# Optimization experiments

Hardware: AMD Instinct MI355X
Metric: run time of the kernel (lower is better)

## Reference

```python
import jax, jax.numpy as jnp
import numpy as np

NC = 1      # constants.nc (Game-of-Life grid channels)
GRID = 32
PAD_ITERS = 31


def _iterated_wrap_idx(n, p):
    # Faithfully simulate p iterations of circular pad-1 on a growing axis.
    # NOTE: this is NOT a single wrap-pad of p; the border alternates 0/n-1.
    idx = np.arange(n)
    for _ in range(p):
        idx = np.concatenate([idx[-1:], idx, idx[:1]])
    return jnp.asarray(idx)

_IDX = _iterated_wrap_idx(GRID, PAD_ITERS)  # length 94, static


def _pad(x):
    # one gather per spatial dim replaces the 31-iteration concat loop
    return x[:, :, _IDX][:, :, :, _IDX]


def _conv(x, w, b, stride):
    y = jax.lax.conv_general_dilated(
        x, w, window_strides=(stride, stride), padding='VALID',
        dimension_numbers=('NCHW', 'OIHW', 'NCHW'))
    return y + b[None, :, None, None]


def setup_inputs() -> dict:
    key = jax.random.key(0)
    ks = jax.random.split(key, 7)
    B = 16
    s_in = 1.0 / np.sqrt(NC * 32 * 32)      # fan-in init, keeps activations sane
    s_hid = 1.0 / np.sqrt(32 * 32 * 32)
    s_out = 1.0 / np.sqrt(32)
    return {
        'x': jax.random.normal(ks[0], (B, NC, GRID, GRID), jnp.float32),
        'in_w': jax.random.normal(ks[1], (32, NC, 32, 32), jnp.float32) * s_in,
        'in_b': jnp.zeros((32,), jnp.float32),
        'convs_w': jax.random.normal(ks[2], (20, 32, 32, 32, 32), jnp.float32) * s_hid,
        'convs_b': jnp.zeros((20, 32), jnp.float32),
        'out_w': jax.random.normal(ks[3], (NC, 32, 1, 1), jnp.float32) * s_out,
        'out_b': jnp.zeros((NC,), jnp.float32),
    }


def reference(x, in_w, in_b, convs_w, convs_b, out_w, out_b):
    # in_conv: pad(31 iters) + conv k=32 s=2 (no ReLU, as in original)
    h = _conv(_pad(x), in_w, in_b, 2)           # [B,32,32,32]

    def step(h, wb):
        w, b = wb
        h = jax.nn.relu(_conv(_pad(h), w, b, 2))
        return h, None

    h, _ = jax.lax.scan(step, h, (convs_w, convs_b))  # 20 hidden layers
    return _conv(h, out_w, out_b, 1)             # 1x1 out conv, no activation
```

## Files before the change

kernel.cpp:

```cpp
#include <hip/hip_runtime.h>


typedef _Float16 f16;
typedef _Float16 f16x8 __attribute__((ext_vector_type(8)));
typedef float f32x4 __attribute__((ext_vector_type(4)));
typedef float f32x16 __attribute__((ext_vector_type(16)));

__device__ __forceinline__ int mwrap(int j) {
  int t = j - 31;
  if ((unsigned)t <= 31u) return t;
  if (t < 0) return (j & 1) ? 0 : 31;
  return (j & 1) ? 0 : 31;
}


template <int CIN, bool RELU, bool PRE>
__global__ __launch_bounds__(512, 2) void gemm3(
    const void* __restrict__ Wv,
    const f16* __restrict__ hp_in,
    const float* __restrict__ bias,
    f16* __restrict__ hp_out) {
  __shared__ __align__(16) f16 rowbuf[2][32][96];
  __shared__ float Red[8][2][1024];

  const int tid = threadIdx.x;
  const int lane = tid & 63;
  const int w = tid >> 6;
  const int ox = lane & 31;
  const int s = lane >> 5;

  const int pair0 = blockIdx.x * 2;
  const int b = pair0 >> 5;
  const int oy0 = pair0 & 31;

  const int rrow = tid / 12, rseg = tid - rrow * 12;

  f32x16 acc0 = {}, acc1 = {};
  f16x8 Acur[8], Anxt[8];
  f16x8 stg = {};

  auto loadA = [&](int c, f16x8* dst) {
#pragma unroll
    for (int kyi = 0; kyi < 4; ++kyi) {
#pragma unroll
      for (int kxh = 0; kxh < 2; ++kxh) {
        const int ky = w + 8 * kyi;
        const int chunk = (c * 32 + ky) * 2 + kxh;
        if constexpr (PRE) {
          const f16* Wl = (const f16*)Wv;
          dst[kyi * 2 + kxh] = *(const f16x8*)(Wl + (size_t)chunk * 512 + lane * 8);
        } else {
          const float* Wl = (const float*)Wv;
          const float* sp = Wl + (((size_t)(ox * CIN + c) * 32 + ky) * 32 + kxh * 16 + s * 8);
          f32x4 u0 = *(const f32x4*)sp;
          f32x4 u1 = *(const f32x4*)(sp + 4);
          f16x8 v;
          v[0] = (f16)u0[0]; v[1] = (f16)u0[1]; v[2] = (f16)u0[2]; v[3] = (f16)u0[3];
          v[4] = (f16)u1[0]; v[5] = (f16)u1[1]; v[6] = (f16)u1[2]; v[7] = (f16)u1[3];
          dst[kyi * 2 + kxh] = v;
        }
      }
    }
  };
  auto loadRow = [&](int c) {
    if (tid < 384)
      stg = *(const f16x8*)(hp_in + ((size_t)(b * CIN + c) * 32 + rrow) * 96 + rseg * 8);
  };
  auto writeRow = [&](int nb) {
    if (tid < 384) *(f16x8*)(&rowbuf[nb][rrow][rseg * 8]) = stg;
  };

  loadA(0, Acur);
  loadRow(0);
  writeRow(0);
  __syncthreads();

  for (int c = 0; c < CIN; ++c) {
    const int buf = c & 1;
    if (c + 1 < CIN) {
      loadA(c + 1, Anxt);
      loadRow(c + 1);
    }
#pragma unroll
    for (int kyi = 0; kyi < 4; ++kyi) {
      const int ky = w + 8 * kyi;
      const int y0 = mwrap(2 * oy0 + ky);
      const int y1 = mwrap(2 * (oy0 + 1) + ky);
      const int* R0 = (const int*)(&rowbuf[buf][y0][0]);
      const int* R1 = (const int*)(&rowbuf[buf][y1][0]);
#pragma unroll
      for (int kxh = 0; kxh < 2; ++kxh) {
        const int bi = ox + 4 * s + 8 * kxh;
        int4 b0w, b1w;
        b0w.x = R0[bi]; b0w.y = R0[bi + 1]; b0w.z = R0[bi + 2]; b0w.w = R0[bi + 3];
        b1w.x = R1[bi]; b1w.y = R1[bi + 1]; b1w.z = R1[bi + 2]; b1w.w = R1[bi + 3];
        f16x8 bf0 = __builtin_bit_cast(f16x8, b0w);
        f16x8 bf1 = __builtin_bit_cast(f16x8, b1w);
        const f16x8 a = Acur[kyi * 2 + kxh];
        acc0 = __builtin_amdgcn_mfma_f32_32x32x16_f16(a, bf0, acc0, 0, 0, 0);
        acc1 = __builtin_amdgcn_mfma_f32_32x32x16_f16(a, bf1, acc1, 0, 0, 0);
      }
    }
    if (c + 1 < CIN) {
      writeRow(buf ^ 1);
#pragma unroll
      for (int u = 0; u < 8; ++u) Acur[u] = Anxt[u];
    }
    __syncthreads();
  }

#pragma unroll
  for (int r = 0; r < 16; ++r) {
    Red[w][0][r * 64 + lane] = acc0[r];
    Red[w][1][r * 64 + lane] = acc1[r];
  }
  __syncthreads();

#pragma unroll
  for (int k4 = 0; k4 < 4; ++k4) {
    const int o = tid + 512 * k4;
    const int p = o >> 10, co = (o >> 5) & 31, oxx = o & 31;
    const int idx = ((co & 3) + 4 * (co >> 3)) * 64 + ((co >> 2) & 1) * 32 + oxx;
    float v = bias[co];
#pragma unroll
    for (int w8 = 0; w8 < 8; ++w8) v += Red[w8][p][idx];
    if (RELU) v = fmaxf(v, 0.f);
    const f16 hv = (f16)v;
    f16* base = hp_out + ((size_t)(b * 32 + co) * 32 + (oy0 + p)) * 96;
    base[oxx + 31] = hv;
    if (oxx == 0) {
#pragma unroll
      for (int j = 1; j <= 29; j += 2) base[j] = hv;
#pragma unroll
      for (int j = 63; j <= 93; j += 2) base[j] = hv;
    }
    if (oxx == 31) {
#pragma unroll
      for (int j = 0; j <= 30; j += 2) base[j] = hv;
#pragma unroll
      for (int j = 64; j <= 92; j += 2) base[j] = hv;
    }
  }
}

__global__ void pad_x_kernel(const float* __restrict__ x, f16* __restrict__ xp) {
  const int i = blockIdx.x * 256 + threadIdx.x;
  if (i >= 48128) return;
  const int bq = i / 3008, r = i - bq * 3008;
  const int y = r / 94, j = r - y * 94;
  xp[bq * 3072 + y * 96 + j] = (f16)x[(bq * 32 + y) * 32 + mwrap(j)];
}

__global__ void convert_w3(const float* __restrict__ in_w,
                           const float* __restrict__ convs_w,
                           f16* __restrict__ WfIn, f16* __restrict__ WfH) {
  const int total = 4096 + 20 * 131072;
  for (int g = blockIdx.x * blockDim.x + threadIdx.x; g < total;
       g += gridDim.x * blockDim.x) {
    const float* src;
    f16* dst;
    int chunk, lanE, c, ky, kxh;
    if (g < 4096) {
      chunk = g >> 6; lanE = g & 63;
      kxh = chunk & 1; ky = chunk >> 1; c = 0;
      const int co = lanE & 31, ss = lanE >> 5;
      src = in_w + ((size_t)(co * 1 + 0) * 32 + ky) * 32 + kxh * 16 + ss * 8;
      dst = WfIn + (size_t)chunk * 512 + lanE * 8;
    } else {
      const int h = g - 4096;
      const int layer = h >> 17, r = h & 131071;
      chunk = r >> 6; lanE = r & 63;
      kxh = chunk & 1;
      const int t = chunk >> 1;
      ky = t & 31; c = t >> 5;
      const int co = lanE & 31, ss = lanE >> 5;
      src = convs_w + (size_t)layer * 1048576 +
            ((size_t)(co * 32 + c) * 32 + ky) * 32 + kxh * 16 + ss * 8;
      dst = WfH + (size_t)layer * 1048576 + (size_t)chunk * 512 + lanE * 8;
    }
    f32x4 u0 = *(const f32x4*)src;
    f32x4 u1 = *(const f32x4*)(src + 4);
    f16x8 v;
    v[0] = (f16)u0[0]; v[1] = (f16)u0[1]; v[2] = (f16)u0[2]; v[3] = (f16)u0[3];
    v[4] = (f16)u1[0]; v[5] = (f16)u1[1]; v[6] = (f16)u1[2]; v[7] = (f16)u1[3];
    *(f16x8*)dst = v;
  }
}

__global__ void out_conv3(const f16* __restrict__ hp,
                          const float* __restrict__ ow,
                          const float* __restrict__ ob,
                          float* __restrict__ out) {
  const int o = blockIdx.x * 256 + threadIdx.x;
  const int b = o >> 10, oy = (o >> 5) & 31, oxx = o & 31;
  float s = ob[0];
#pragma unroll
  for (int c = 0; c < 32; ++c)
    s += ow[c] * (float)hp[((size_t)(b * 32 + c) * 32 + oy) * 96 + oxx + 31];
  out[o] = s;
}

extern "C" void kernel_launch(void* const* d_in, const int* in_sizes, int n_in,
                              void* d_out, int out_size, void* d_ws,
                              size_t ws_size, hipStream_t stream) {
  const float* x = (const float*)d_in[0];
  const float* in_w = (const float*)d_in[1];
  const float* in_b = (const float*)d_in[2];
  const float* convs_w = (const float*)d_in[3];
  const float* convs_b = (const float*)d_in[4];
  const float* out_w = (const float*)d_in[5];
  const float* out_b = (const float*)d_in[6];
  float* out = (float*)d_out;

  char* ws = (char*)d_ws;
  f16* xpad = (f16*)ws;
  f16* hpA = (f16*)(ws + 98304);
  f16* hpB = (f16*)(ws + 98304 + 3145728);
  f16* WfIn = (f16*)(ws + 6389760);
  f16* WfH = (f16*)(ws + 6455296);
  const bool pre = (ws_size >= 48398336ull);

  pad_x_kernel<<<188, 256, 0, stream>>>(x, xpad);
  if (pre) convert_w3<<<2048, 256, 0, stream>>>(in_w, convs_w, WfIn, WfH);

  if (pre)
    gemm3<1, false, true><<<256, 512, 0, stream>>>(WfIn, xpad, in_b, hpA);
  else
    gemm3<1, false, false><<<256, 512, 0, stream>>>(in_w, xpad, in_b, hpA);

  for (int l = 0; l < 20; ++l) {
    const f16* cur = (l % 2 == 0) ? hpA : hpB;
    f16* nxt = (l % 2 == 0) ? hpB : hpA;
    if (pre)
      gemm3<32, true, true><<<256, 512, 0, stream>>>(
          WfH + (size_t)l * 1048576, cur, convs_b + 32 * l, nxt);
    else
      gemm3<32, true, false><<<256, 512, 0, stream>>>(
          convs_w + (size_t)l * 1048576, cur, convs_b + 32 * l, nxt);
  }

  out_conv3<<<64, 256, 0, stream>>>(hpA, out_w, out_b, out);
}
```

Baseline: 1.022 ms.

## Regroup kernel rows per warp, pre-shift LDS planes, and process two channels per barrier

Each warp now owns four contiguous kernel rows instead of rows strided by eight. That lets the two output rows share overlapping input rows, so six fragments replace eight per half. The input rows are staged into LDS as four pre-shifted copies, so every B fragment becomes one aligned 16-byte LDS read instead of four scalar reads. Two input channels are staged and computed per barrier, which halves the synchronisations. The cost is a much larger LDS footprint (about 98 KB, reused for the reduction), more staging stores and more register use.

```diff
diff --git a/kernel.cpp b/kernel.cpp
--- a/kernel.cpp
+++ b/kernel.cpp
@@ -13,106 +13,136 @@
   return (j & 1) ? 0 : 31;
 }
 
+#define PLANE 3080
+#define CHST 12320
+#define BUFST 24640
 
 template <int CIN, bool RELU, bool PRE>
-__global__ __launch_bounds__(512, 2) void gemm3(
-    const void* __restrict__ Wv,
-    const f16* __restrict__ hp_in,
-    const float* __restrict__ bias,
-    f16* __restrict__ hp_out) {
-  __shared__ __align__(16) f16 rowbuf[2][32][96];
-  __shared__ float Red[8][2][1024];
+__global__ __launch_bounds__(512, 2) void gemm4(
+    const void* __restrict__ Wv, const f16* __restrict__ hp_in,
+    const float* __restrict__ bias, f16* __restrict__ hp_out) {
+  __shared__ __align__(16) char smem[98560];
+  f16* Sw = (f16*)smem;
+  float* Red = (float*)smem;
 
   const int tid = threadIdx.x;
   const int lane = tid & 63;
   const int w = tid >> 6;
   const int ox = lane & 31;
   const int s = lane >> 5;
-
   const int pair0 = blockIdx.x * 2;
   const int b = pair0 >> 5;
   const int oy0 = pair0 & 31;
 
-  const int rrow = tid / 12, rseg = tid - rrow * 12;
+  const int bi0 = ox + 4 * s;
+  const int r = (4 - (bi0 & 3)) & 3;
+  const int m0 = (bi0 + r) >> 2;
+  int fragOff[6];
+#pragma unroll
+  for (int t = 0; t < 6; ++t)
+    fragOff[t] = r * PLANE + mwrap(2 * oy0 + 4 * w + t) * 96 + m0 * 8;
+
+  int stgLds[6], stgG[6], stgCh[6];
+#pragma unroll
+  for (int k = 0; k < 6; ++k) {
+    const int id = k * 512 + tid;
+    const int ch = id / 1536, rem = id - ch * 1536;
+    const int cp = rem / 384, rem2 = rem - cp * 384;
+    const int y = rem2 / 12, u = rem2 - y * 12;
+    stgCh[k] = ch;
+    stgLds[k] = ch * CHST + cp * PLANE + y * 96 + u * 8;
+    stgG[k] = ch * 3072 + y * 96 + (u * 8 - cp * 2);
+  }
+  const f16* gbase = hp_in + (size_t)b * CIN * 3072;
 
   f32x16 acc0 = {}, acc1 = {};
-  f16x8 Acur[8], Anxt[8];
-  f16x8 stg = {};
-
-  auto loadA = [&](int c, f16x8* dst) {
-#pragma unroll
-    for (int kyi = 0; kyi < 4; ++kyi) {
-#pragma unroll
-      for (int kxh = 0; kxh < 2; ++kxh) {
-        const int ky = w + 8 * kyi;
-        const int chunk = (c * 32 + ky) * 2 + kxh;
-        if constexpr (PRE) {
-          const f16* Wl = (const f16*)Wv;
-          dst[kyi * 2 + kxh] = *(const f16x8*)(Wl + (size_t)chunk * 512 + lane * 8);
-        } else {
-          const float* Wl = (const float*)Wv;
-          const float* sp = Wl + (((size_t)(ox * CIN + c) * 32 + ky) * 32 + kxh * 16 + s * 8);
+  f16x8 Ac[2][8], An[2][8];
+  int stgi[6][4];
+
+  auto loadA = [&](int c, f16x8(&dst)[8]) {
+    if constexpr (PRE) {
+      const f16* base = (const f16*)Wv + (size_t)(c * 64 + 8 * w) * 512 + lane * 8;
+#pragma unroll
+      for (int u = 0; u < 8; ++u) dst[u] = *(const f16x8*)(base + u * 512);
+    } else {
+      const float* W = (const float*)Wv;
+#pragma unroll
+      for (int i = 0; i < 4; ++i)
+#pragma unroll
+        for (int kxh = 0; kxh < 2; ++kxh) {
+          const float* sp =
+              W + ((size_t)(ox * CIN + c) * 32 + (4 * w + i)) * 32 + kxh * 16 + s * 8;
           f32x4 u0 = *(const f32x4*)sp;
           f32x4 u1 = *(const f32x4*)(sp + 4);
           f16x8 v;
           v[0] = (f16)u0[0]; v[1] = (f16)u0[1]; v[2] = (f16)u0[2]; v[3] = (f16)u0[3];
           v[4] = (f16)u1[0]; v[5] = (f16)u1[1]; v[6] = (f16)u1[2]; v[7] = (f16)u1[3];
-          dst[kyi * 2 + kxh] = v;
+          dst[i * 2 + kxh] = v;
         }
+    }
+  };
+  auto loadStg = [&](int c0) {
+    const f16* gp = gbase + (size_t)c0 * 3072;
+#pragma unroll
+    for (int k = 0; k < 6; ++k)
+      if (c0 + stgCh[k] < CIN) {
+#pragma unroll
+        for (int d = 0; d < 4; ++d) stgi[k][d] = *(const int*)(gp + stgG[k] + 2 * d);
       }
-    }
-  };
-  auto loadRow = [&](int c) {
-    if (tid < 384)
-      stg = *(const f16x8*)(hp_in + ((size_t)(b * CIN + c) * 32 + rrow) * 96 + rseg * 8);
-  };
-  auto writeRow = [&](int nb) {
-    if (tid < 384) *(f16x8*)(&rowbuf[nb][rrow][rseg * 8]) = stg;
-  };
-
-  loadA(0, Acur);
-  loadRow(0);
-  writeRow(0);
+  };
+  auto writeStg = [&](int buf) {
+#pragma unroll
+    for (int k = 0; k < 6; ++k) {
+      int4 v;
+      v.x = stgi[k][0]; v.y = stgi[k][1]; v.z = stgi[k][2]; v.w = stgi[k][3];
+      *(int4*)(Sw + buf * BUFST + stgLds[k]) = v;
+    }
+  };
+  auto compute = [&](int buf, f16x8(&A)[8], int ch) {
+    const f16* Sb = Sw + buf * BUFST + ch * CHST;
+#pragma unroll
+    for (int kxh = 0; kxh < 2; ++kxh) {
+      f16x8 F[6];
+#pragma unroll
+      for (int t = 0; t < 6; ++t) F[t] = *(const f16x8*)(Sb + fragOff[t] + kxh * 16);
+#pragma unroll
+      for (int i = 0; i < 4; ++i) {
+        acc0 = __builtin_amdgcn_mfma_f32_32x32x16_f16(A[i * 2 + kxh], F[i], acc0, 0, 0, 0);
+        acc1 = __builtin_amdgcn_mfma_f32_32x32x16_f16(A[i * 2 + kxh], F[i + 2], acc1, 0, 0, 0);
+      }
+    }
+  };
+
+  constexpr int G = (CIN + 1) / 2;
+  loadA(0, Ac[0]);
+  if (CIN > 1) loadA(1, Ac[1]);
+  loadStg(0);
+  writeStg(0);
   __syncthreads();
 
-  for (int c = 0; c < CIN; ++c) {
-    const int buf = c & 1;
-    if (c + 1 < CIN) {
-      loadA(c + 1, Anxt);
-      loadRow(c + 1);
-    }
-#pragma unroll
-    for (int kyi = 0; kyi < 4; ++kyi) {
-      const int ky = w + 8 * kyi;
-      const int y0 = mwrap(2 * oy0 + ky);
-      const int y1 = mwrap(2 * (oy0 + 1) + ky);
-      const int* R0 = (const int*)(&rowbuf[buf][y0][0]);
-      const int* R1 = (const int*)(&rowbuf[buf][y1][0]);
-#pragma unroll
-      for (int kxh = 0; kxh < 2; ++kxh) {
-        const int bi = ox + 4 * s + 8 * kxh;
-        int4 b0w, b1w;
-        b0w.x = R0[bi]; b0w.y = R0[bi + 1]; b0w.z = R0[bi + 2]; b0w.w = R0[bi + 3];
-        b1w.x = R1[bi]; b1w.y = R1[bi + 1]; b1w.z = R1[bi + 2]; b1w.w = R1[bi + 3];
-        f16x8 bf0 = __builtin_bit_cast(f16x8, b0w);
-        f16x8 bf1 = __builtin_bit_cast(f16x8, b1w);
-        const f16x8 a = Acur[kyi * 2 + kxh];
-        acc0 = __builtin_amdgcn_mfma_f32_32x32x16_f16(a, bf0, acc0, 0, 0, 0);
-        acc1 = __builtin_amdgcn_mfma_f32_32x32x16_f16(a, bf1, acc1, 0, 0, 0);
-      }
-    }
-    if (c + 1 < CIN) {
-      writeRow(buf ^ 1);
-#pragma unroll
-      for (int u = 0; u < 8; ++u) Acur[u] = Anxt[u];
+  for (int g = 0; g < G; ++g) {
+    const int buf = g & 1;
+    if (g + 1 < G) {
+      loadA(2 * g + 2, An[0]);
+      loadA(2 * g + 3, An[1]);
+      loadStg(2 * g + 2);
+    }
+    compute(buf, Ac[0], 0);
+    if (2 * g + 1 < CIN) compute(buf, Ac[1], 1);
+    if (g + 1 < G) {
+      writeStg(buf ^ 1);
+#pragma unroll
+      for (int ch = 0; ch < 2; ++ch)
+#pragma unroll
+        for (int u = 0; u < 8; ++u) Ac[ch][u] = An[ch][u];
     }
     __syncthreads();
   }
 
 #pragma unroll
-  for (int r = 0; r < 16; ++r) {
-    Red[w][0][r * 64 + lane] = acc0[r];
-    Red[w][1][r * 64 + lane] = acc1[r];
+  for (int rr = 0; rr < 16; ++rr) {
+    Red[w * 2048 + rr * 64 + lane] = acc0[rr];
+    Red[w * 2048 + 1024 + rr * 64 + lane] = acc1[rr];
   }
   __syncthreads();
 
@@ -123,7 +153,7 @@
     const int idx = ((co & 3) + 4 * (co >> 3)) * 64 + ((co >> 2) & 1) * 32 + oxx;
     float v = bias[co];
 #pragma unroll
-    for (int w8 = 0; w8 < 8; ++w8) v += Red[w8][p][idx];
+    for (int w8 = 0; w8 < 8; ++w8) v += Red[w8 * 2048 + p * 1024 + idx];
     if (RELU) v = fmaxf(v, 0.f);
     const f16 hv = (f16)v;
     f16* base = hp_out + ((size_t)(b * 32 + co) * 32 + (oy0 + p)) * 96;
@@ -164,7 +194,7 @@
       chunk = g >> 6; lanE = g & 63;
       kxh = chunk & 1; ky = chunk >> 1; c = 0;
       const int co = lanE & 31, ss = lanE >> 5;
-      src = in_w + ((size_t)(co * 1 + 0) * 32 + ky) * 32 + kxh * 16 + ss * 8;
+      src = in_w + ((size_t)co * 32 + ky) * 32 + kxh * 16 + ss * 8;
       dst = WfIn + (size_t)chunk * 512 + lanE * 8;
     } else {
       const int h = g - 4096;
@@ -213,29 +243,29 @@
   float* out = (float*)d_out;
 
   char* ws = (char*)d_ws;
-  f16* xpad = (f16*)ws;
-  f16* hpA = (f16*)(ws + 98304);
-  f16* hpB = (f16*)(ws + 98304 + 3145728);
-  f16* WfIn = (f16*)(ws + 6389760);
-  f16* WfH = (f16*)(ws + 6455296);
-  const bool pre = (ws_size >= 48398336ull);
+  f16* xpad = (f16*)(ws + 256);
+  f16* hpA = (f16*)(ws + 256 + 98304);
+  f16* hpB = (f16*)(ws + 256 + 98304 + 3145728);
+  f16* WfIn = (f16*)(ws + 6390016);
+  f16* WfH = (f16*)(ws + 6455552);
+  const bool pre = (ws_size >= 48398592ull);
 
   pad_x_kernel<<<188, 256, 0, stream>>>(x, xpad);
   if (pre) convert_w3<<<2048, 256, 0, stream>>>(in_w, convs_w, WfIn, WfH);
 
   if (pre)
-    gemm3<1, false, true><<<256, 512, 0, stream>>>(WfIn, xpad, in_b, hpA);
+    gemm4<1, false, true><<<256, 512, 0, stream>>>(WfIn, xpad, in_b, hpA);
   else
-    gemm3<1, false, false><<<256, 512, 0, stream>>>(in_w, xpad, in_b, hpA);
+    gemm4<1, false, false><<<256, 512, 0, stream>>>(in_w, xpad, in_b, hpA);
 
   for (int l = 0; l < 20; ++l) {
     const f16* cur = (l % 2 == 0) ? hpA : hpB;
     f16* nxt = (l % 2 == 0) ? hpB : hpA;
     if (pre)
-      gemm3<32, true, true><<<256, 512, 0, stream>>>(
+      gemm4<32, true, true><<<256, 512, 0, stream>>>(
           WfH + (size_t)l * 1048576, cur, convs_b + 32 * l, nxt);
     else
-      gemm3<32, true, false><<<256, 512, 0, stream>>>(
+      gemm4<32, true, false><<<256, 512, 0, stream>>>(
           convs_w + (size_t)l * 1048576, cur, convs_b + 32 * l, nxt);
   }
 
```

Result: slower. 1.064 ms (+4.2%).

## Split-K conv layers across blocks with atomic fp32 accumulation and deferred ReLU

Applied to the files above, without the earlier changes.

Replaces the per-row-pair GEMM with a split-K design. Each block handles one batch image over a slice of input channels (or ky rows for the input conv), computes all 32 output rows, and accumulates partial sums into an fp32 buffer with atomicAdd. ReLU and f16 conversion move to the consumer's load, and padding is done on the fly in shared memory, so the separate pad kernel and padded f16 buffers go away. Weights are double-buffered through LDS by phases, and B rows are reused across a sliding register window. The cost is memset launches per layer, atomic traffic, and fp32 activations in place of f16.

```diff
diff --git a/kernel.cpp b/kernel.cpp
--- a/kernel.cpp
+++ b/kernel.cpp
@@ -9,146 +9,159 @@
 __device__ __forceinline__ int mwrap(int j) {
   int t = j - 31;
   if ((unsigned)t <= 31u) return t;
-  if (t < 0) return (j & 1) ? 0 : 31;
   return (j & 1) ? 0 : 31;
 }
 
-
-template <int CIN, bool RELU, bool PRE>
-__global__ __launch_bounds__(512, 2) void gemm3(
-    const void* __restrict__ Wv,
-    const f16* __restrict__ hp_in,
+#define BROW 104
+
+template <int NPH, int KYPP, bool RELUIN, bool PRE, bool INCONV>
+__global__ __launch_bounds__(512, 2) void gemm5(
+    const f16* __restrict__ Wf,
+    const float* __restrict__ Wraw,
+    const float* __restrict__ src,
     const float* __restrict__ bias,
-    f16* __restrict__ hp_out) {
-  __shared__ __align__(16) f16 rowbuf[2][32][96];
-  __shared__ float Red[8][2][1024];
+    float* __restrict__ dst) {
+  constexpr int NCH = INCONV ? 1 : (NPH * KYPP / 32);
+  constexpr int SLICES = INCONV ? 4 : 16;
+  constexpr int ABYTES = KYPP * 2048;
+  constexpr int UPT = KYPP / 4;
+  constexpr int CINW = INCONV ? 1 : 32;
+
+  __shared__ __align__(16) char smem[2 * ABYTES + NCH * 32 * BROW * 2 + 16];
+  f16* Bsh = (f16*)(smem + 2 * ABYTES);
 
   const int tid = threadIdx.x;
   const int lane = tid & 63;
   const int w = tid >> 6;
   const int ox = lane & 31;
-  const int s = lane >> 5;
-
-  const int pair0 = blockIdx.x * 2;
-  const int b = pair0 >> 5;
-  const int oy0 = pair0 & 31;
-
-  const int rrow = tid / 12, rseg = tid - rrow * 12;
-
-  f32x16 acc0 = {}, acc1 = {};
-  f16x8 Acur[8], Anxt[8];
-  f16x8 stg = {};
-
-  auto loadA = [&](int c, f16x8* dst) {
-#pragma unroll
-    for (int kyi = 0; kyi < 4; ++kyi) {
+  const int sl = lane >> 5;
+  const int oy0 = w * 4;
+  const int sli = blockIdx.x & (SLICES - 1);
+  const int b = blockIdx.x / SLICES;
+  const int c0 = INCONV ? 0 : 2 * sli;
+  const int ky0 = INCONV ? 8 * sli : 0;
+
+  const f16* Wsl = Wf + ((size_t)(c0 * 32 + ky0) << 10);
+
+  {
+    const int NB = NCH * 384;
+    for (int base = 0; base < NB; base += 512) {
+      const int id = base + tid;
+      if (id < NB) {
+        const int cl = id / 384, rem = id % 384;
+        const int y = rem / 12, u9 = rem % 12;
+        const float* sp = src + (((size_t)b * CINW + c0 + cl) * 32 + y) * 32;
+        f16x8 v;
+#pragma unroll
+        for (int i = 0; i < 8; ++i) {
+          float t = sp[mwrap(u9 * 8 + i)];
+          if (RELUIN) t = fmaxf(t, 0.f);
+          v[i] = (f16)t;
+        }
+        *(f16x8*)(Bsh + (cl * 32 + y) * BROW + u9 * 8) = v;
+      }
+    }
+  }
+
+  int4 pf[UPT];
+  auto prefA = [&](int ph1) {
+    if constexpr (PRE) {
+      const char* gp = (const char*)Wsl + (size_t)ph1 * ABYTES;
+#pragma unroll
+      for (int u = 0; u < UPT; ++u)
+        pf[u] = *(const int4*)(gp + (u * 512 + tid) * 16);
+    } else {
+#pragma unroll
+      for (int u = 0; u < UPT; ++u) {
+        const int e = (u * 512 + tid) * 8;
+        const int chk = e >> 9, li = (e >> 3) & 63;
+        const int co = li & 31, ss = li >> 5;
+        const int kk = chk >> 1, kxh = chk & 1;
+        const int g = ph1 * KYPP + kk;
+        const int cl = g >> 5, kyg = ky0 + (g & 31);
+        const float* sp = Wraw + (((size_t)co * CINW + c0 + cl) * 32 + kyg) * 32 +
+                          kxh * 16 + ss * 8;
+        f32x4 a0 = *(const f32x4*)sp;
+        f32x4 a1 = *(const f32x4*)(sp + 4);
+        f16x8 v;
+        v[0] = (f16)a0[0]; v[1] = (f16)a0[1]; v[2] = (f16)a0[2]; v[3] = (f16)a0[3];
+        v[4] = (f16)a1[0]; v[5] = (f16)a1[1]; v[6] = (f16)a1[2]; v[7] = (f16)a1[3];
+        pf[u] = __builtin_bit_cast(int4, v);
+      }
+    }
+  };
+  auto wrA = [&](int nb) {
+    char* lp = smem + nb * ABYTES;
+#pragma unroll
+    for (int u = 0; u < UPT; ++u)
+      *(int4*)(lp + (u * 512 + tid) * 16) = pf[u];
+  };
+
+  prefA(0);
+  wrA(0);
+  __syncthreads();
+
+  f32x16 acc[4] = {};
+  f16x8 Bw[2][4][2];
+  const int Rbase = ox + 4 * sl;
+
+  auto loadB = [&](int cloc, int j, int kxh) -> f16x8 {
+    const int y = mwrap(j);
+    const int* R = (const int*)Bsh + (cloc * 32 + y) * (BROW / 2) + Rbase + 8 * kxh;
+    int4 t;
+    t.x = R[0]; t.y = R[1]; t.z = R[2]; t.w = R[3];
+    return __builtin_bit_cast(f16x8, t);
+  };
+
+  for (int ph = 0; ph < NPH; ++ph) {
+    if (ph + 1 < NPH) prefA(ph + 1);
+    const char* Ab = smem + (ph & 1) * ABYTES;
+#pragma unroll
+    for (int kk = 0; kk < KYPP; ++kk) {
+      const int g = ph * KYPP + kk;
+      const int cloc = g >> 5;
+      const int ky = ky0 + (g & 31);
+      const int p = g & 1;
+      const int J0 = 2 * oy0 + ky;
+      if ((g & 31) < 2) {
+#pragma unroll
+        for (int t = 0; t < 4; ++t) {
+          Bw[p][t][0] = loadB(cloc, J0 + 2 * t, 0);
+          Bw[p][t][1] = loadB(cloc, J0 + 2 * t, 1);
+        }
+      } else {
+#pragma unroll
+        for (int t = 0; t < 3; ++t) {
+          Bw[p][t][0] = Bw[p][t + 1][0];
+          Bw[p][t][1] = Bw[p][t + 1][1];
+        }
+        Bw[p][3][0] = loadB(cloc, J0 + 6, 0);
+        Bw[p][3][1] = loadB(cloc, J0 + 6, 1);
+      }
 #pragma unroll
       for (int kxh = 0; kxh < 2; ++kxh) {
-        const int ky = w + 8 * kyi;
-        const int chunk = (c * 32 + ky) * 2 + kxh;
-        if constexpr (PRE) {
-          const f16* Wl = (const f16*)Wv;
-          dst[kyi * 2 + kxh] = *(const f16x8*)(Wl + (size_t)chunk * 512 + lane * 8);
-        } else {
-          const float* Wl = (const float*)Wv;
-          const float* sp = Wl + (((size_t)(ox * CIN + c) * 32 + ky) * 32 + kxh * 16 + s * 8);
-          f32x4 u0 = *(const f32x4*)sp;
-          f32x4 u1 = *(const f32x4*)(sp + 4);
-          f16x8 v;
-          v[0] = (f16)u0[0]; v[1] = (f16)u0[1]; v[2] = (f16)u0[2]; v[3] = (f16)u0[3];
-          v[4] = (f16)u1[0]; v[5] = (f16)u1[1]; v[6] = (f16)u1[2]; v[7] = (f16)u1[3];
-          dst[kyi * 2 + kxh] = v;
-        }
-      }
-    }
-  };
-  auto loadRow = [&](int c) {
-    if (tid < 384)
-      stg = *(const f16x8*)(hp_in + ((size_t)(b * CIN + c) * 32 + rrow) * 96 + rseg * 8);
-  };
-  auto writeRow = [&](int nb) {
-    if (tid < 384) *(f16x8*)(&rowbuf[nb][rrow][rseg * 8]) = stg;
-  };
-
-  loadA(0, Acur);
-  loadRow(0);
-  writeRow(0);
-  __syncthreads();
-
-  for (int c = 0; c < CIN; ++c) {
-    const int buf = c & 1;
-    if (c + 1 < CIN) {
-      loadA(c + 1, Anxt);
-      loadRow(c + 1);
-    }
-#pragma unroll
-    for (int kyi = 0; kyi < 4; ++kyi) {
-      const int ky = w + 8 * kyi;
-      const int y0 = mwrap(2 * oy0 + ky);
-      const int y1 = mwrap(2 * (oy0 + 1) + ky);
-      const int* R0 = (const int*)(&rowbuf[buf][y0][0]);
-      const int* R1 = (const int*)(&rowbuf[buf][y1][0]);
-#pragma unroll
-      for (int kxh = 0; kxh < 2; ++kxh) {
-        const int bi = ox + 4 * s + 8 * kxh;
-        int4 b0w, b1w;
-        b0w.x = R0[bi]; b0w.y = R0[bi + 1]; b0w.z = R0[bi + 2]; b0w.w = R0[bi + 3];
-        b1w.x = R1[bi]; b1w.y = R1[bi + 1]; b1w.z = R1[bi + 2]; b1w.w = R1[bi + 3];
-        f16x8 bf0 = __builtin_bit_cast(f16x8, b0w);
-        f16x8 bf1 = __builtin_bit_cast(f16x8, b1w);
-        const f16x8 a = Acur[kyi * 2 + kxh];
-        acc0 = __builtin_amdgcn_mfma_f32_32x32x16_f16(a, bf0, acc0, 0, 0, 0);
-        acc1 = __builtin_amdgcn_mfma_f32_32x32x16_f16(a, bf1, acc1, 0, 0, 0);
-      }
-    }
-    if (c + 1 < CIN) {
-      writeRow(buf ^ 1);
-#pragma unroll
-      for (int u = 0; u < 8; ++u) Acur[u] = Anxt[u];
-    }
+        f16x8 a = *(const f16x8*)(Ab + (kk * 2 + kxh) * 1024 + lane * 16);
+#pragma unroll
+        for (int t = 0; t < 4; ++t)
+          acc[t] = __builtin_amdgcn_mfma_f32_32x32x16_f16(a, Bw[p][t][kxh], acc[t], 0, 0, 0);
+      }
+    }
+    if (ph + 1 < NPH) wrA((ph + 1) & 1);
     __syncthreads();
   }
 
-#pragma unroll
-  for (int r = 0; r < 16; ++r) {
-    Red[w][0][r * 64 + lane] = acc0[r];
-    Red[w][1][r * 64 + lane] = acc1[r];
-  }
-  __syncthreads();
-
-#pragma unroll
-  for (int k4 = 0; k4 < 4; ++k4) {
-    const int o = tid + 512 * k4;
-    const int p = o >> 10, co = (o >> 5) & 31, oxx = o & 31;
-    const int idx = ((co & 3) + 4 * (co >> 3)) * 64 + ((co >> 2) & 1) * 32 + oxx;
-    float v = bias[co];
-#pragma unroll
-    for (int w8 = 0; w8 < 8; ++w8) v += Red[w8][p][idx];
-    if (RELU) v = fmaxf(v, 0.f);
-    const f16 hv = (f16)v;
-    f16* base = hp_out + ((size_t)(b * 32 + co) * 32 + (oy0 + p)) * 96;
-    base[oxx + 31] = hv;
-    if (oxx == 0) {
-#pragma unroll
-      for (int j = 1; j <= 29; j += 2) base[j] = hv;
-#pragma unroll
-      for (int j = 63; j <= 93; j += 2) base[j] = hv;
-    }
-    if (oxx == 31) {
-#pragma unroll
-      for (int j = 0; j <= 30; j += 2) base[j] = hv;
-#pragma unroll
-      for (int j = 64; j <= 92; j += 2) base[j] = hv;
-    }
-  }
-}
-
-__global__ void pad_x_kernel(const float* __restrict__ x, f16* __restrict__ xp) {
-  const int i = blockIdx.x * 256 + threadIdx.x;
-  if (i >= 48128) return;
-  const int bq = i / 3008, r = i - bq * 3008;
-  const int y = r / 94, j = r - y * 94;
-  xp[bq * 3072 + y * 96 + j] = (f16)x[(bq * 32 + y) * 32 + mwrap(j)];
+  const bool sliceZero = (sli == 0);
+#pragma unroll
+  for (int t = 0; t < 4; ++t) {
+    const int oy = oy0 + t;
+#pragma unroll
+    for (int r = 0; r < 16; ++r) {
+      const int co = (r & 3) + 8 * (r >> 2) + 4 * sl;
+      float v = acc[t][r];
+      if (sliceZero) v += bias[co];
+      atomicAdd(dst + (((size_t)b * 32 + co) * 32 + oy) * 32 + ox, v);
+    }
+  }
 }
 
 __global__ void convert_w3(const float* __restrict__ in_w,
@@ -164,7 +177,7 @@
       chunk = g >> 6; lanE = g & 63;
       kxh = chunk & 1; ky = chunk >> 1; c = 0;
       const int co = lanE & 31, ss = lanE >> 5;
-      src = in_w + ((size_t)(co * 1 + 0) * 32 + ky) * 32 + kxh * 16 + ss * 8;
+      src = in_w + ((size_t)co * 32 + ky) * 32 + kxh * 16 + ss * 8;
       dst = WfIn + (size_t)chunk * 512 + lanE * 8;
     } else {
       const int h = g - 4096;
@@ -187,16 +200,16 @@
   }
 }
 
-__global__ void out_conv3(const f16* __restrict__ hp,
+__global__ void out_conv5(const float* __restrict__ hb,
                           const float* __restrict__ ow,
                           const float* __restrict__ ob,
                           float* __restrict__ out) {
   const int o = blockIdx.x * 256 + threadIdx.x;
-  const int b = o >> 10, oy = (o >> 5) & 31, oxx = o & 31;
+  const int b = o >> 10, rem = o & 1023;
   float s = ob[0];
 #pragma unroll
   for (int c = 0; c < 32; ++c)
-    s += ow[c] * (float)hp[((size_t)(b * 32 + c) * 32 + oy) * 96 + oxx + 31];
+    s += ow[c] * fmaxf(hb[((size_t)b * 32 + c) * 1024 + rem], 0.f);
   out[o] = s;
 }
 
@@ -213,31 +226,41 @@
   float* out = (float*)d_out;
 
   char* ws = (char*)d_ws;
-  f16* xpad = (f16*)ws;
-  f16* hpA = (f16*)(ws + 98304);
-  f16* hpB = (f16*)(ws + 98304 + 3145728);
-  f16* WfIn = (f16*)(ws + 6389760);
-  f16* WfH = (f16*)(ws + 6455296);
-  const bool pre = (ws_size >= 48398336ull);
-
-  pad_x_kernel<<<188, 256, 0, stream>>>(x, xpad);
+  const size_t BUF = 2097152;
+  float* bufA = (float*)ws;
+  float* bufB = (float*)(ws + BUF);
+  f16* WfIn = (f16*)(ws + 2 * BUF);
+  f16* WfH = (f16*)(ws + 2 * BUF + 65536);
+  const bool pre = (ws_size >= 2 * BUF + 65536 + 41943040ull);
+
+  hipMemsetAsync(bufA, 0, BUF, stream);
+  hipMemsetAsync(bufB, 0, BUF, stream);
   if (pre) convert_w3<<<2048, 256, 0, stream>>>(in_w, convs_w, WfIn, WfH);
 
   if (pre)
-    gemm3<1, false, true><<<256, 512, 0, stream>>>(WfIn, xpad, in_b, hpA);
+    gemm5<1, 8, false, true, true><<<64, 512, 0, stream>>>(WfIn, in_w, x, in_b, bufA);
   else
-    gemm3<1, false, false><<<256, 512, 0, stream>>>(in_w, xpad, in_b, hpA);
+    gemm5<1, 8, false, false, true><<<64, 512, 0, stream>>>(WfIn, in_w, x, in_b, bufA);
 
   for (int l = 0; l < 20; ++l) {
-    const f16* cur = (l % 2 == 0) ? hpA : hpB;
-    f16* nxt = (l % 2 == 0) ? hpB : hpA;
-    if (pre)
-      gemm3<32, true, true><<<256, 512, 0, stream>>>(
-          WfH + (size_t)l * 1048576, cur, convs_b + 32 * l, nxt);
-    else
-      gemm3<32, true, false><<<256, 512, 0, stream>>>(
-          convs_w + (size_t)l * 1048576, cur, convs_b + 32 * l, nxt);
-  }
-
-  out_conv3<<<64, 256, 0, stream>>>(hpA, out_w, out_b, out);
-}
+    const float* cur = (l & 1) ? bufB : bufA;
+    float* nxt = (l & 1) ? bufA : bufB;
+    if (l >= 1) hipMemsetAsync(nxt, 0, BUF, stream);
+    const f16* Wl = WfH + (size_t)l * 1048576;
+    const float* Wr = convs_w + (size_t)l * 1048576;
+    const float* bs = convs_b + 32 * l;
+    if (pre) {
+      if (l == 0)
+        gemm5<4, 16, false, true, false><<<256, 512, 0, stream>>>(Wl, Wr, cur, bs, nxt);
+      else
+        gemm5<4, 16, true, true, false><<<256, 512, 0, stream>>>(Wl, Wr, cur, bs, nxt);
+    } else {
+      if (l == 0)
+        gemm5<4, 16, false, false, false><<<256, 512, 0, stream>>>(Wl, Wr, cur, bs, nxt);
+      else
+        gemm5<4, 16, true, false, false><<<256, 512, 0, stream>>>(Wl, Wr, cur, bs, nxt);
+    }
+  }
+
+  out_conv5<<<64, 256, 0, stream>>>(bufA, out_w, out_b, out);
+}
```

After: 1.536 ms. +50.4%, slower.
